# Optimization experiments

Hardware: AMD Instinct MI355X
Metric: run time of the kernel (lower is better)

The kernel has to match this reference:

```python
import jax, jax.numpy as jnp
import numpy as np

N_VEH, N_PED = 16, 16
DV, DP = 40, 24            # vehicle / pedestrian slot obs dims
N = N_VEH + N_PED          # 32 agents
E, H = 128, 4              # embed_dim, num_heads
DH = E // H                # head_dim = 32
B = 4096
OBS = N_VEH * DV + N_PED * DP + N  # 1056


def setup_inputs() -> dict:
    key = jax.random.key(0)
    ks = jax.random.split(key, 12)
    s = lambda fan_in: 1.0 / np.sqrt(fan_in)
    inp = {
        "global_obs": jax.random.uniform(ks[0], (B, OBS), dtype=jnp.float32),
        # per-type projectors (stored as (in, out) so x @ W + b)
        "Wv": jax.random.uniform(ks[1], (DV, E), jnp.float32, -s(DV), s(DV)),
        "bv": jax.random.uniform(ks[2], (E,), jnp.float32, -s(DV), s(DV)),
        "Wp": jax.random.uniform(ks[3], (DP, E), jnp.float32, -s(DP), s(DP)),
        "bp": jax.random.uniform(ks[4], (E,), jnp.float32, -s(DP), s(DP)),
        # GAT layer 0 / 1: w (E, H*DH), a_src / a_dst (H, DH)
        "w0": jax.random.normal(ks[5], (E, H * DH), jnp.float32) * s(E),
        "asrc0": jax.random.normal(ks[6], (H, DH), jnp.float32) * s(DH),
        "adst0": jax.random.normal(ks[7], (H, DH), jnp.float32) * s(DH),
        "w1": jax.random.normal(ks[8], (E, H * DH), jnp.float32) * s(E),
        "asrc1": jax.random.normal(ks[9], (H, DH), jnp.float32) * s(DH),
        "adst1": jax.random.normal(ks[10], (H, DH), jnp.float32) * s(DH),
    }
    return inp


def _gat(x, alive, w, a_src, a_dst):
    # x: (B,N,E), alive: (B,N) in {0,1}
    b, n, _ = x.shape
    h = (x @ w).reshape(b, n, H, DH)                       # (B,N,H,DH)
    alpha_src = jnp.einsum("bnhd,hd->bnh", h, a_src)       # (B,N,H)
    alpha_dst = jnp.einsum("bnhd,hd->bnh", h, a_dst)
    e = alpha_src[:, :, None, :] + alpha_dst[:, None, :, :]  # (B,Ni,Nj,H)
    e = jnp.where(e > 0, e, 0.2 * e)                       # LeakyReLU(0.2)
    key_mask = alive[:, None, :, None] >= 0.5              # mask over j
    e = jnp.where(key_mask, e, -jnp.inf)
    attn = jax.nn.softmax(e, axis=2)                       # softmax over keys j
    attn = jnp.nan_to_num(attn)
    out = jnp.einsum("bijh,bjhd->bihd", attn, h)           # weighted aggregate
    return out.reshape(b, n, H * DH)                       # concat heads


def reference(global_obs, Wv, bv, Wp, bp, w0, asrc0, adst0, w1, asrc1, adst1):
    b = global_obs.shape[0]
    veh = global_obs[:, : N_VEH * DV].reshape(b, N_VEH, DV)
    ped = global_obs[:, N_VEH * DV : N_VEH * DV + N_PED * DP].reshape(b, N_PED, DP)
    alive_raw = global_obs[:, -N:]
    tokens = jnp.concatenate([veh @ Wv + bv, ped @ Wp + bp], axis=1)  # (B,N,E)
    alive = (alive_raw >= 0.5).astype(jnp.float32)
    all_dead = jnp.sum(alive, axis=1, keepdims=True) < 0.5
    alive = jnp.where(all_dead, jnp.ones_like(alive), alive)
    x = tokens
    for (w, a_s, a_d) in ((w0, asrc0, adst0), (w1, asrc1, adst1)):
        x = jax.nn.elu(_gat(x, alive, w, a_s, a_d))
    aw = alive[:, :, None]
    pooled = jnp.sum(x * aw, axis=1) / jnp.clip(jnp.sum(aw, axis=1), 1.0)
    return pooled
```

## Files before the change

### kernel.cpp

```cpp
#include <hip/hip_runtime.h>


#define NTOK 32
#define EMB  128
#define OBSL 1056
#define XSTR 136
#define HSTR 40
#define TILE 5120

typedef __attribute__((ext_vector_type(8))) short  short8;
typedef __attribute__((ext_vector_type(4))) float  floatx4;
typedef __attribute__((ext_vector_type(2))) unsigned uint2v;

__device__ __forceinline__ short f2bf(float f) {
  union { float f; unsigned u; } v; v.f = f;
  unsigned r = (v.u + 0x7fffu + ((v.u >> 16) & 1u)) >> 16;
  return (short)(unsigned short)r;
}
__device__ __forceinline__ unsigned pk2(float a, float b) {
  unsigned r; asm("v_cvt_pk_bf16_f32 %0, %1, %2" : "=v"(r) : "v"(a), "v"(b)); return r;
}
__device__ __forceinline__ float exp2_hw(float x) {
#if __has_builtin(__builtin_amdgcn_exp2f)
  return __builtin_amdgcn_exp2f(x);
#else
  return exp2f(x);
#endif
}
__device__ __forceinline__ float rcp_hw(float x) {
#if __has_builtin(__builtin_amdgcn_rcpf)
  return __builtin_amdgcn_rcpf(x);
#else
  return 1.0f / x;
#endif
}
__device__ __forceinline__ float elu1(float v) { return v > 0.f ? v : __expf(v) - 1.f; }
__device__ __forceinline__ floatx4 mfma16(short8 a, short8 b, floatx4 c) {
  return __builtin_amdgcn_mfma_f32_16x16x32_bf16(a, b, c, 0, 0, 0);
}

__global__ void prep_weights(const float* __restrict__ Wv, const float* __restrict__ Wp,
                             const float* __restrict__ w0, const float* __restrict__ w1,
                             short* __restrict__ ws) {
  int idx = blockIdx.x * 256 + threadIdx.x;
  if (idx < 8192) {
    int e = idx >> 6, k = idx & 63;
    float v = (k < 40) ? Wv[(size_t)k * EMB + e] : Wp[(size_t)(k - 40) * EMB + e];
    ws[idx] = f2bf(v);
  } else if (idx < 24576) {
    int t = idx - 8192; int e = t >> 7, k = t & 127;
    ws[idx] = f2bf(w0[(size_t)k * EMB + e]);
  } else {
    int t = idx - 24576; int e = t >> 7, k = t & 127;
    ws[idx] = f2bf(w1[(size_t)k * EMB + e]);
  }
}

__global__ __launch_bounds__(256, 6) void gnn_fused(
    const float* __restrict__ obs,
    const float* __restrict__ bv, const float* __restrict__ bp,
    const float* __restrict__ as0, const float* __restrict__ ad0,
    const float* __restrict__ as1, const float* __restrict__ ad1,
    const short* __restrict__ wsb,
    float* __restrict__ out)
{
  __shared__ __align__(16) short s_t[TILE];

  const int tid  = threadIdx.x;
  const int lane = tid & 63;
  const int wv   = tid >> 6;
  const int col  = lane & 15;
  const int quad = lane >> 4;
  const int b    = blockIdx.x;

  const float* orow = obs + (size_t)b * OBSL;
  short* xbase = s_t;
  short* hbase = &s_t[wv * 1280];
  const short8  z8 = {0,0,0,0,0,0,0,0};
  const floatx4 fz = {0.f,0.f,0.f,0.f};

  float flag; float invc;
  {
    float araw = (lane < NTOK) ? orow[1024 + lane] : 0.f;
    bool alv = (lane < NTOK) && (araw >= 0.5f);
    unsigned long long m = __ballot(alv);
    int cnt = __popcll(m);
    flag = alv ? 1.f : 0.f;
    if (cnt == 0) { flag = (lane < NTOK) ? 1.f : 0.f; cnt = NTOK; }
    invc = 1.f / (float)cnt;
  }
  const float alvI0 = __shfl(flag, col);
  const float alvI1 = __shfl(flag, 16 + col);

  {
    int c = wv * 64 + lane;
    *(short8*)&xbase[(c >> 3) * XSTR + (c & 7) * 8] = z8;
  }
  __syncthreads();
  {
    int i4 = wv * 64 + lane;
    float4 v = *(const float4*)&orow[i4 * 4];
    int r, k;
    if (i4 < 160) { r = (i4 * 205) >> 11;  k = (i4 - r * 10) * 4; }
    else { int t2 = i4 - 160; int q6 = (t2 * 171) >> 10; r = 16 + q6; k = 40 + (t2 - q6 * 6) * 4; }
    uint2v u; u.x = pk2(v.x, v.y); u.y = pk2(v.z, v.w);
    *(uint2v*)&xbase[r * XSTR + k] = u;
  }
  __syncthreads();

  {
    short8 Bxin[2][2];
    #pragma unroll
    for (int nt = 0; nt < 2; ++nt)
      #pragma unroll
      for (int kt = 0; kt < 2; ++kt)
        Bxin[nt][kt] = *(const short8*)&xbase[(nt * 16 + col) * XSTR + kt * 32 + quad * 8];
    __syncthreads();
    const short* embT = wsb;
    #pragma unroll
    for (int mi = 0; mi < 2; ++mi) {
      const int mtE = wv * 2 + mi;
      short8 A0 = *(const short8*)&embT[(mtE * 16 + col) * 64 + quad * 8];
      short8 A1 = *(const short8*)&embT[(mtE * 16 + col) * 64 + 32 + quad * 8];
      float4 bv4 = *(const float4*)&bv[mtE * 16 + quad * 4];
      float4 bp4 = *(const float4*)&bp[mtE * 16 + quad * 4];
      #pragma unroll
      for (int nt = 0; nt < 2; ++nt) {
        floatx4 acc = fz;
        acc = mfma16(A0, Bxin[nt][0], acc);
        acc = mfma16(A1, Bxin[nt][1], acc);
        float4 bb = nt ? bp4 : bv4;
        uint2v u; u.x = pk2(acc[0] + bb.x, acc[1] + bb.y); u.y = pk2(acc[2] + bb.z, acc[3] + bb.w);
        *(uint2v*)&xbase[(nt * 16 + col) * XSTR + mtE * 16 + quad * 4] = u;
      }
    }
  }

  for (int L = 0; L < 2; ++L) {
    const short* wT  = wsb + 8192 + L * 16384;
    const float* gas = L ? as1 : as0;
    const float* gad = L ? ad1 : ad0;

    __syncthreads();

    floatx4 acc[2][2];
    #pragma unroll
    for (int mi = 0; mi < 2; ++mi) { acc[mi][0] = fz; acc[mi][1] = fz; }
    #pragma unroll
    for (int kt = 0; kt < 4; ++kt) {
      short8 B0 = *(const short8*)&xbase[(col) * XSTR + kt * 32 + quad * 8];
      short8 B1 = *(const short8*)&xbase[(16 + col) * XSTR + kt * 32 + quad * 8];
      #pragma unroll
      for (int mi = 0; mi < 2; ++mi) {
        const int mt = wv * 2 + mi;
        short8 A = *(const short8*)&wT[(mt * 16 + col) * 128 + kt * 32 + quad * 8];
        acc[mi][0] = mfma16(A, B0, acc[mi][0]);
        acc[mi][1] = mfma16(A, B1, acc[mi][1]);
      }
    }

    float psrc[2], pdst[2];
    psrc[0] = 0.f; psrc[1] = 0.f; pdst[0] = 0.f; pdst[1] = 0.f;
    #pragma unroll
    for (int mi = 0; mi < 2; ++mi) {
      const int mt = wv * 2 + mi;
      float4 cs = *(const float4*)&gas[mt * 16 + quad * 4];
      float4 cd = *(const float4*)&gad[mt * 16 + quad * 4];
      #pragma unroll
      for (int nt = 0; nt < 2; ++nt) {
        floatx4 a = acc[mi][nt];
        psrc[nt] += a[0]*cs.x + a[1]*cs.y + a[2]*cs.z + a[3]*cs.w;
        pdst[nt] += a[0]*cd.x + a[1]*cd.y + a[2]*cd.z + a[3]*cd.w;
      }
    }
    __syncthreads();

    #pragma unroll
    for (int mi = 0; mi < 2; ++mi) {
      const int rowloc = mi * 16 + quad * 4;
      #pragma unroll
      for (int nt = 0; nt < 2; ++nt) {
        floatx4 a = acc[mi][nt];
        unsigned u01 = pk2(a[0], a[1]);
        unsigned u23 = pk2(a[2], a[3]);
        unsigned short* hrow = (unsigned short*)&hbase[rowloc * HSTR + nt * 16 + col];
        hrow[0]        = (unsigned short)u01;
        hrow[HSTR]     = (unsigned short)(u01 >> 16);
        hrow[2 * HSTR] = (unsigned short)u23;
        hrow[3 * HSTR] = (unsigned short)(u23 >> 16);
      }
    }

    #pragma unroll
    for (int nt = 0; nt < 2; ++nt) {
      float vs = psrc[nt]; vs += __shfl_xor(vs, 16); vs += __shfl_xor(vs, 32);
      psrc[nt] = vs * 1.44269504088896340736f;
      float vd = pdst[nt]; vd += __shfl_xor(vd, 16); vd += __shfl_xor(vd, 32);
      pdst[nt] = vd * 1.44269504088896340736f;
    }

    float alv8[8];
    #pragma unroll
    for (int jj = 0; jj < 8; ++jj) alv8[jj] = __shfl(flag, quad * 8 + jj);

    short8 pf[2];
    {
      float vsel = (quad >> 1) ? pdst[1] : pdst[0];
      float ad8[8];
      #pragma unroll
      for (int jj = 0; jj < 8; ++jj) {
        float v = __shfl(vsel, ((quad >> 1) << 5) + ((quad & 1) << 3) + jj);
        ad8[jj] = (alv8[jj] >= 0.5f) ? v : -1e30f;
      }
      #pragma unroll
      for (int ii = 0; ii < 2; ++ii) {
        float ai = psrc[ii];
        float ev[8]; float sum = 0.f;
        #pragma unroll
        for (int jj = 0; jj < 8; ++jj) {
          float e = ai + ad8[jj];
          e = fmaxf(e, 0.2f * e);
          float p = exp2_hw(e);
          ev[jj] = p; sum += p;
        }
        sum += __shfl_xor(sum, 16);
        sum += __shfl_xor(sum, 32);
        float inv = rcp_hw(sum);
        union { unsigned u4[4]; short8 s; } pu;
        #pragma unroll
        for (int p2 = 0; p2 < 4; ++p2) pu.u4[p2] = pk2(ev[2*p2] * inv, ev[2*p2+1] * inv);
        pf[ii] = pu.s;
      }
    }

    short8 Ah[2];
    #pragma unroll
    for (int mt2 = 0; mt2 < 2; ++mt2)
      Ah[mt2] = *(const short8*)&hbase[(mt2 * 16 + col) * HSTR + quad * 8];
    if (L == 0) __syncthreads();

    #pragma unroll
    for (int mt2 = 0; mt2 < 2; ++mt2) {
      floatx4 po[2];
      #pragma unroll
      for (int nt = 0; nt < 2; ++nt) {
        po[nt] = mfma16(Ah[mt2], pf[nt], fz);
      }
      const int ecol = wv * 32 + mt2 * 16 + quad * 4;
      if (L == 0) {
        #pragma unroll
        for (int nt = 0; nt < 2; ++nt) {
          uint2v u;
          u.x = pk2(elu1(po[nt][0]), elu1(po[nt][1]));
          u.y = pk2(elu1(po[nt][2]), elu1(po[nt][3]));
          *(uint2v*)&xbase[(nt * 16 + col) * XSTR + ecol] = u;
        }
      } else {
        #pragma unroll
        for (int r = 0; r < 4; ++r) {
          float s = elu1(po[0][r]) * alvI0 + elu1(po[1][r]) * alvI1;
          s += __shfl_xor(s, 1); s += __shfl_xor(s, 2);
          s += __shfl_xor(s, 4); s += __shfl_xor(s, 8);
          if (col == 0) out[(size_t)b * EMB + ecol + r] = s * invc;
        }
      }
    }
  }
}

extern "C" void kernel_launch(void* const* d_in, const int* in_sizes, int n_in,
                              void* d_out, int out_size, void* d_ws, size_t ws_size,
                              hipStream_t stream) {
  const float* obs = (const float*)d_in[0];
  const float* Wv  = (const float*)d_in[1];
  const float* bv  = (const float*)d_in[2];
  const float* Wp  = (const float*)d_in[3];
  const float* bp  = (const float*)d_in[4];
  const float* w0  = (const float*)d_in[5];
  const float* as0 = (const float*)d_in[6];
  const float* ad0 = (const float*)d_in[7];
  const float* w1  = (const float*)d_in[8];
  const float* as1 = (const float*)d_in[9];
  const float* ad1 = (const float*)d_in[10];
  float* out = (float*)d_out;
  short* wsb = (short*)d_ws;

  int Bn = in_sizes[0] / OBSL;
  prep_weights<<<160, 256, 0, stream>>>(Wv, Wp, w0, w1, wsb);
  gnn_fused<<<Bn, 256, 0, stream>>>(obs, bv, bp, as0, ad0, as1, ad1, wsb, out);
}
```

Measured before the change: 130.2 us.

## Process two batch samples per block to reuse weight fragments

Each block now handles two batch rows with a doubled shared tile, so the weight A-fragments loaded from global memory are reused across both samples in the embedding and GAT matmuls. Alive flags become a 32-bit mask in place of per-lane floats and shuffles, and the zero-fill only touches the padding regions. The grid is halved, which raises register and LDS pressure per block and may lower occupancy under the 6-blocks launch bound. It also assumes an even batch size.

```diff
diff --git a/kernel.cpp b/kernel.cpp
--- a/kernel.cpp
+++ b/kernel.cpp
@@ -64,57 +64,62 @@
     const short* __restrict__ wsb,
     float* __restrict__ out)
 {
-  __shared__ __align__(16) short s_t[TILE];
+  __shared__ __align__(16) short s_t[2][TILE];
 
   const int tid  = threadIdx.x;
   const int lane = tid & 63;
   const int wv   = tid >> 6;
   const int col  = lane & 15;
   const int quad = lane >> 4;
-  const int b    = blockIdx.x;
-
-  const float* orow = obs + (size_t)b * OBSL;
-  short* xbase = s_t;
-  short* hbase = &s_t[wv * 1280];
+  const size_t b0 = (size_t)blockIdx.x * 2;
+
   const short8  z8 = {0,0,0,0,0,0,0,0};
   const floatx4 fz = {0.f,0.f,0.f,0.f};
 
-  float flag; float invc;
-  {
+  unsigned m32[2]; float invc[2];
+  #pragma unroll
+  for (int j = 0; j < 2; ++j) {
+    const float* orow = obs + (b0 + j) * OBSL;
     float araw = (lane < NTOK) ? orow[1024 + lane] : 0.f;
     bool alv = (lane < NTOK) && (araw >= 0.5f);
     unsigned long long m = __ballot(alv);
     int cnt = __popcll(m);
-    flag = alv ? 1.f : 0.f;
-    if (cnt == 0) { flag = (lane < NTOK) ? 1.f : 0.f; cnt = NTOK; }
-    invc = 1.f / (float)cnt;
-  }
-  const float alvI0 = __shfl(flag, col);
-  const float alvI1 = __shfl(flag, 16 + col);
+    unsigned mm = (unsigned)m;
+    if (cnt == 0) { mm = 0xFFFFFFFFu; cnt = NTOK; }
+    m32[j] = mm; invc[j] = 1.f / (float)cnt;
+  }
 
   {
-    int c = wv * 64 + lane;
-    *(short8*)&xbase[(c >> 3) * XSTR + (c & 7) * 8] = z8;
-  }
-  __syncthreads();
-  {
+    int idx = tid; int r = -1, k = 0;
+    if (idx < 48)       { r = (idx * 171) >> 9;  k = 40 + (idx - r * 3) * 8; }
+    else if (idx < 128) { int t2 = idx - 48; int q5 = (t2 * 205) >> 10; r = 16 + q5; k = (t2 - q5 * 5) * 8; }
+    if (r >= 0) {
+      *(short8*)&s_t[0][r * XSTR + k] = z8;
+      *(short8*)&s_t[1][r * XSTR + k] = z8;
+    }
+  }
+  #pragma unroll
+  for (int j = 0; j < 2; ++j) {
+    const float* orow = obs + (b0 + j) * OBSL;
     int i4 = wv * 64 + lane;
     float4 v = *(const float4*)&orow[i4 * 4];
     int r, k;
     if (i4 < 160) { r = (i4 * 205) >> 11;  k = (i4 - r * 10) * 4; }
     else { int t2 = i4 - 160; int q6 = (t2 * 171) >> 10; r = 16 + q6; k = 40 + (t2 - q6 * 6) * 4; }
     uint2v u; u.x = pk2(v.x, v.y); u.y = pk2(v.z, v.w);
-    *(uint2v*)&xbase[r * XSTR + k] = u;
+    *(uint2v*)&s_t[j][r * XSTR + k] = u;
   }
   __syncthreads();
 
   {
-    short8 Bxin[2][2];
-    #pragma unroll
-    for (int nt = 0; nt < 2; ++nt)
-      #pragma unroll
-      for (int kt = 0; kt < 2; ++kt)
-        Bxin[nt][kt] = *(const short8*)&xbase[(nt * 16 + col) * XSTR + kt * 32 + quad * 8];
+    short8 Bxin[2][2][2];
+    #pragma unroll
+    for (int j = 0; j < 2; ++j)
+      #pragma unroll
+      for (int nt = 0; nt < 2; ++nt)
+        #pragma unroll
+        for (int kt = 0; kt < 2; ++kt)
+          Bxin[j][nt][kt] = *(const short8*)&s_t[j][(nt * 16 + col) * XSTR + kt * 32 + quad * 8];
     __syncthreads();
     const short* embT = wsb;
     #pragma unroll
@@ -125,14 +130,16 @@
       float4 bv4 = *(const float4*)&bv[mtE * 16 + quad * 4];
       float4 bp4 = *(const float4*)&bp[mtE * 16 + quad * 4];
       #pragma unroll
-      for (int nt = 0; nt < 2; ++nt) {
-        floatx4 acc = fz;
-        acc = mfma16(A0, Bxin[nt][0], acc);
-        acc = mfma16(A1, Bxin[nt][1], acc);
-        float4 bb = nt ? bp4 : bv4;
-        uint2v u; u.x = pk2(acc[0] + bb.x, acc[1] + bb.y); u.y = pk2(acc[2] + bb.z, acc[3] + bb.w);
-        *(uint2v*)&xbase[(nt * 16 + col) * XSTR + mtE * 16 + quad * 4] = u;
-      }
+      for (int j = 0; j < 2; ++j)
+        #pragma unroll
+        for (int nt = 0; nt < 2; ++nt) {
+          floatx4 acc = fz;
+          acc = mfma16(A0, Bxin[j][nt][0], acc);
+          acc = mfma16(A1, Bxin[j][nt][1], acc);
+          float4 bb = nt ? bp4 : bv4;
+          uint2v u; u.x = pk2(acc[0] + bb.x, acc[1] + bb.y); u.y = pk2(acc[2] + bb.z, acc[3] + bb.w);
+          *(uint2v*)&s_t[j][(nt * 16 + col) * XSTR + mtE * 16 + quad * 4] = u;
+        }
     }
   }
 
@@ -143,78 +150,88 @@
 
     __syncthreads();
 
-    floatx4 acc[2][2];
-    #pragma unroll
-    for (int mi = 0; mi < 2; ++mi) { acc[mi][0] = fz; acc[mi][1] = fz; }
+    floatx4 acc[2][2][2];
+    #pragma unroll
+    for (int j = 0; j < 2; ++j)
+      #pragma unroll
+      for (int mi = 0; mi < 2; ++mi) { acc[j][mi][0] = fz; acc[j][mi][1] = fz; }
     #pragma unroll
     for (int kt = 0; kt < 4; ++kt) {
-      short8 B0 = *(const short8*)&xbase[(col) * XSTR + kt * 32 + quad * 8];
-      short8 B1 = *(const short8*)&xbase[(16 + col) * XSTR + kt * 32 + quad * 8];
-      #pragma unroll
-      for (int mi = 0; mi < 2; ++mi) {
-        const int mt = wv * 2 + mi;
-        short8 A = *(const short8*)&wT[(mt * 16 + col) * 128 + kt * 32 + quad * 8];
-        acc[mi][0] = mfma16(A, B0, acc[mi][0]);
-        acc[mi][1] = mfma16(A, B1, acc[mi][1]);
-      }
-    }
-
-    float psrc[2], pdst[2];
-    psrc[0] = 0.f; psrc[1] = 0.f; pdst[0] = 0.f; pdst[1] = 0.f;
+      #pragma unroll
+      for (int j = 0; j < 2; ++j) {
+        short8 B0 = *(const short8*)&s_t[j][(col) * XSTR + kt * 32 + quad * 8];
+        short8 B1 = *(const short8*)&s_t[j][(16 + col) * XSTR + kt * 32 + quad * 8];
+        #pragma unroll
+        for (int mi = 0; mi < 2; ++mi) {
+          const int mt = wv * 2 + mi;
+          short8 A = *(const short8*)&wT[(mt * 16 + col) * 128 + kt * 32 + quad * 8];
+          acc[j][mi][0] = mfma16(A, B0, acc[j][mi][0]);
+          acc[j][mi][1] = mfma16(A, B1, acc[j][mi][1]);
+        }
+      }
+    }
+
+    float psrc[2][2], pdst[2][2];
+    #pragma unroll
+    for (int j = 0; j < 2; ++j) { psrc[j][0]=0.f; psrc[j][1]=0.f; pdst[j][0]=0.f; pdst[j][1]=0.f; }
     #pragma unroll
     for (int mi = 0; mi < 2; ++mi) {
       const int mt = wv * 2 + mi;
       float4 cs = *(const float4*)&gas[mt * 16 + quad * 4];
       float4 cd = *(const float4*)&gad[mt * 16 + quad * 4];
       #pragma unroll
+      for (int j = 0; j < 2; ++j)
+        #pragma unroll
+        for (int nt = 0; nt < 2; ++nt) {
+          floatx4 a = acc[j][mi][nt];
+          psrc[j][nt] += a[0]*cs.x + a[1]*cs.y + a[2]*cs.z + a[3]*cs.w;
+          pdst[j][nt] += a[0]*cd.x + a[1]*cd.y + a[2]*cd.z + a[3]*cd.w;
+        }
+    }
+    __syncthreads();
+
+    #pragma unroll
+    for (int j = 0; j < 2; ++j)
+      #pragma unroll
+      for (int mi = 0; mi < 2; ++mi) {
+        const int rowloc = mi * 16 + quad * 4;
+        #pragma unroll
+        for (int nt = 0; nt < 2; ++nt) {
+          floatx4 a = acc[j][mi][nt];
+          unsigned u01 = pk2(a[0], a[1]);
+          unsigned u23 = pk2(a[2], a[3]);
+          unsigned short* hrow = (unsigned short*)&s_t[j][wv * 1280 + rowloc * HSTR + nt * 16 + col];
+          hrow[0]        = (unsigned short)u01;
+          hrow[HSTR]     = (unsigned short)(u01 >> 16);
+          hrow[2 * HSTR] = (unsigned short)u23;
+          hrow[3 * HSTR] = (unsigned short)(u23 >> 16);
+        }
+      }
+
+    #pragma unroll
+    for (int j = 0; j < 2; ++j)
+      #pragma unroll
       for (int nt = 0; nt < 2; ++nt) {
-        floatx4 a = acc[mi][nt];
-        psrc[nt] += a[0]*cs.x + a[1]*cs.y + a[2]*cs.z + a[3]*cs.w;
-        pdst[nt] += a[0]*cd.x + a[1]*cd.y + a[2]*cd.z + a[3]*cd.w;
-      }
-    }
-    __syncthreads();
-
-    #pragma unroll
-    for (int mi = 0; mi < 2; ++mi) {
-      const int rowloc = mi * 16 + quad * 4;
-      #pragma unroll
-      for (int nt = 0; nt < 2; ++nt) {
-        floatx4 a = acc[mi][nt];
-        unsigned u01 = pk2(a[0], a[1]);
-        unsigned u23 = pk2(a[2], a[3]);
-        unsigned short* hrow = (unsigned short*)&hbase[rowloc * HSTR + nt * 16 + col];
-        hrow[0]        = (unsigned short)u01;
-        hrow[HSTR]     = (unsigned short)(u01 >> 16);
-        hrow[2 * HSTR] = (unsigned short)u23;
-        hrow[3 * HSTR] = (unsigned short)(u23 >> 16);
-      }
-    }
-
-    #pragma unroll
-    for (int nt = 0; nt < 2; ++nt) {
-      float vs = psrc[nt]; vs += __shfl_xor(vs, 16); vs += __shfl_xor(vs, 32);
-      psrc[nt] = vs * 1.44269504088896340736f;
-      float vd = pdst[nt]; vd += __shfl_xor(vd, 16); vd += __shfl_xor(vd, 32);
-      pdst[nt] = vd * 1.44269504088896340736f;
-    }
-
-    float alv8[8];
-    #pragma unroll
-    for (int jj = 0; jj < 8; ++jj) alv8[jj] = __shfl(flag, quad * 8 + jj);
-
-    short8 pf[2];
-    {
-      float vsel = (quad >> 1) ? pdst[1] : pdst[0];
+        float vs = psrc[j][nt]; vs += __shfl_xor(vs, 16); vs += __shfl_xor(vs, 32);
+        psrc[j][nt] = vs * 1.44269504088896340736f;
+        float vd = pdst[j][nt]; vd += __shfl_xor(vd, 16); vd += __shfl_xor(vd, 32);
+        pdst[j][nt] = vd * 1.44269504088896340736f;
+      }
+
+    short8 pf[2][2];
+    #pragma unroll
+    for (int j = 0; j < 2; ++j) {
+      float vsel = (quad >> 1) ? pdst[j][1] : pdst[j][0];
       float ad8[8];
       #pragma unroll
       for (int jj = 0; jj < 8; ++jj) {
         float v = __shfl(vsel, ((quad >> 1) << 5) + ((quad & 1) << 3) + jj);
-        ad8[jj] = (alv8[jj] >= 0.5f) ? v : -1e30f;
+        bool alive = (m32[j] >> (quad * 8 + jj)) & 1u;
+        ad8[jj] = alive ? v : -1e30f;
       }
       #pragma unroll
       for (int ii = 0; ii < 2; ++ii) {
-        float ai = psrc[ii];
+        float ai = psrc[j][ii];
         float ev[8]; float sum = 0.f;
         #pragma unroll
         for (int jj = 0; jj < 8; ++jj) {
@@ -229,39 +246,46 @@
         union { unsigned u4[4]; short8 s; } pu;
         #pragma unroll
         for (int p2 = 0; p2 < 4; ++p2) pu.u4[p2] = pk2(ev[2*p2] * inv, ev[2*p2+1] * inv);
-        pf[ii] = pu.s;
-      }
-    }
-
-    short8 Ah[2];
-    #pragma unroll
-    for (int mt2 = 0; mt2 < 2; ++mt2)
-      Ah[mt2] = *(const short8*)&hbase[(mt2 * 16 + col) * HSTR + quad * 8];
+        pf[j][ii] = pu.s;
+      }
+    }
+
+    short8 Ah[2][2];
+    #pragma unroll
+    for (int j = 0; j < 2; ++j)
+      #pragma unroll
+      for (int mt2 = 0; mt2 < 2; ++mt2)
+        Ah[j][mt2] = *(const short8*)&s_t[j][wv * 1280 + (mt2 * 16 + col) * HSTR + quad * 8];
     if (L == 0) __syncthreads();
 
     #pragma unroll
-    for (int mt2 = 0; mt2 < 2; ++mt2) {
-      floatx4 po[2];
-      #pragma unroll
-      for (int nt = 0; nt < 2; ++nt) {
-        po[nt] = mfma16(Ah[mt2], pf[nt], fz);
-      }
-      const int ecol = wv * 32 + mt2 * 16 + quad * 4;
-      if (L == 0) {
+    for (int j = 0; j < 2; ++j) {
+      #pragma unroll
+      for (int mt2 = 0; mt2 < 2; ++mt2) {
+        floatx4 po[2];
         #pragma unroll
         for (int nt = 0; nt < 2; ++nt) {
-          uint2v u;
-          u.x = pk2(elu1(po[nt][0]), elu1(po[nt][1]));
-          u.y = pk2(elu1(po[nt][2]), elu1(po[nt][3]));
-          *(uint2v*)&xbase[(nt * 16 + col) * XSTR + ecol] = u;
-        }
-      } else {
-        #pragma unroll
-        for (int r = 0; r < 4; ++r) {
-          float s = elu1(po[0][r]) * alvI0 + elu1(po[1][r]) * alvI1;
-          s += __shfl_xor(s, 1); s += __shfl_xor(s, 2);
-          s += __shfl_xor(s, 4); s += __shfl_xor(s, 8);
-          if (col == 0) out[(size_t)b * EMB + ecol + r] = s * invc;
+          po[nt] = mfma16(Ah[j][mt2], pf[j][nt], fz);
+        }
+        const int ecol = wv * 32 + mt2 * 16 + quad * 4;
+        if (L == 0) {
+          #pragma unroll
+          for (int nt = 0; nt < 2; ++nt) {
+            uint2v u;
+            u.x = pk2(elu1(po[nt][0]), elu1(po[nt][1]));
+            u.y = pk2(elu1(po[nt][2]), elu1(po[nt][3]));
+            *(uint2v*)&s_t[j][(nt * 16 + col) * XSTR + ecol] = u;
+          }
+        } else {
+          float aI0 = ((m32[j] >> col) & 1u) ? 1.f : 0.f;
+          float aI1 = ((m32[j] >> (16 + col)) & 1u) ? 1.f : 0.f;
+          #pragma unroll
+          for (int r = 0; r < 4; ++r) {
+            float s = elu1(po[0][r]) * aI0 + elu1(po[1][r]) * aI1;
+            s += __shfl_xor(s, 1); s += __shfl_xor(s, 2);
+            s += __shfl_xor(s, 4); s += __shfl_xor(s, 8);
+            if (col == 0) out[(b0 + j) * EMB + ecol + r] = s * invc[j];
+          }
         }
       }
     }
@@ -287,5 +311,5 @@
 
   int Bn = in_sizes[0] / OBSL;
   prep_weights<<<160, 256, 0, stream>>>(Wv, Wp, w0, w1, wsb);
-  gnn_fused<<<Bn, 256, 0, stream>>>(obs, bv, bp, as0, ad0, as1, ad1, wsb, out);
-}
+  gnn_fused<<<Bn / 2, 256, 0, stream>>>(obs, bv, bp, as0, ad0, as1, ad1, wsb, out);
+}
```

Result: no change. 128.8 us (-1.1%).

## Process two batch rows per block with separate x/h shared buffers

Applied to the files above, without the earlier changes.

Each block now loops over two samples, which halves the grid and amortizes block launch overhead. Shared memory is split into separate x and h buffers, so the h-tile writes no longer alias x and one barrier per layer can be dropped. Only the padding columns are zeroed, and the alive flags are kept as a 32-bit bitmask instead of shuffled floats. The two samples are handled one after the other, so per-block latency roughly doubles and fewer blocks are available to hide it; Bn/2 also assumes an even batch size.

```diff
diff --git a/kernel.cpp b/kernel.cpp
--- a/kernel.cpp
+++ b/kernel.cpp
@@ -6,7 +6,6 @@
 #define OBSL 1056
 #define XSTR 136
 #define HSTR 40
-#define TILE 5120
 
 typedef __attribute__((ext_vector_type(8))) short  short8;
 typedef __attribute__((ext_vector_type(4))) float  floatx4;
@@ -64,204 +63,206 @@
     const short* __restrict__ wsb,
     float* __restrict__ out)
 {
-  __shared__ __align__(16) short s_t[TILE];
+  __shared__ __align__(16) short s_x[32 * XSTR];
+  __shared__ __align__(16) short s_h[4 * 32 * HSTR];
 
   const int tid  = threadIdx.x;
   const int lane = tid & 63;
   const int wv   = tid >> 6;
   const int col  = lane & 15;
   const int quad = lane >> 4;
-  const int b    = blockIdx.x;
-
-  const float* orow = obs + (size_t)b * OBSL;
-  short* xbase = s_t;
-  short* hbase = &s_t[wv * 1280];
+
+  short* hbase = &s_h[wv * 1280];
   const short8  z8 = {0,0,0,0,0,0,0,0};
   const floatx4 fz = {0.f,0.f,0.f,0.f};
 
-  float flag; float invc;
-  {
-    float araw = (lane < NTOK) ? orow[1024 + lane] : 0.f;
-    bool alv = (lane < NTOK) && (araw >= 0.5f);
-    unsigned long long m = __ballot(alv);
-    int cnt = __popcll(m);
-    flag = alv ? 1.f : 0.f;
-    if (cnt == 0) { flag = (lane < NTOK) ? 1.f : 0.f; cnt = NTOK; }
-    invc = 1.f / (float)cnt;
-  }
-  const float alvI0 = __shfl(flag, col);
-  const float alvI1 = __shfl(flag, 16 + col);
-
-  {
-    int c = wv * 64 + lane;
-    *(short8*)&xbase[(c >> 3) * XSTR + (c & 7) * 8] = z8;
-  }
-  __syncthreads();
-  {
-    int i4 = wv * 64 + lane;
-    float4 v = *(const float4*)&orow[i4 * 4];
-    int r, k;
-    if (i4 < 160) { r = (i4 * 205) >> 11;  k = (i4 - r * 10) * 4; }
-    else { int t2 = i4 - 160; int q6 = (t2 * 171) >> 10; r = 16 + q6; k = 40 + (t2 - q6 * 6) * 4; }
-    uint2v u; u.x = pk2(v.x, v.y); u.y = pk2(v.z, v.w);
-    *(uint2v*)&xbase[r * XSTR + k] = u;
-  }
-  __syncthreads();
-
-  {
-    short8 Bxin[2][2];
-    #pragma unroll
-    for (int nt = 0; nt < 2; ++nt)
-      #pragma unroll
-      for (int kt = 0; kt < 2; ++kt)
-        Bxin[nt][kt] = *(const short8*)&xbase[(nt * 16 + col) * XSTR + kt * 32 + quad * 8];
+  for (int j = 0; j < 2; ++j) {
+    const size_t b = (size_t)blockIdx.x * 2 + j;
+    const float* orow = obs + b * OBSL;
+
     __syncthreads();
-    const short* embT = wsb;
-    #pragma unroll
-    for (int mi = 0; mi < 2; ++mi) {
-      const int mtE = wv * 2 + mi;
-      short8 A0 = *(const short8*)&embT[(mtE * 16 + col) * 64 + quad * 8];
-      short8 A1 = *(const short8*)&embT[(mtE * 16 + col) * 64 + 32 + quad * 8];
-      float4 bv4 = *(const float4*)&bv[mtE * 16 + quad * 4];
-      float4 bp4 = *(const float4*)&bp[mtE * 16 + quad * 4];
-      #pragma unroll
-      for (int nt = 0; nt < 2; ++nt) {
-        floatx4 acc = fz;
-        acc = mfma16(A0, Bxin[nt][0], acc);
-        acc = mfma16(A1, Bxin[nt][1], acc);
-        float4 bb = nt ? bp4 : bv4;
-        uint2v u; u.x = pk2(acc[0] + bb.x, acc[1] + bb.y); u.y = pk2(acc[2] + bb.z, acc[3] + bb.w);
-        *(uint2v*)&xbase[(nt * 16 + col) * XSTR + mtE * 16 + quad * 4] = u;
-      }
-    }
-  }
-
-  for (int L = 0; L < 2; ++L) {
-    const short* wT  = wsb + 8192 + L * 16384;
-    const float* gas = L ? as1 : as0;
-    const float* gad = L ? ad1 : ad0;
-
+
+    unsigned m32; float invc;
+    {
+      float araw = (lane < NTOK) ? orow[1024 + lane] : 0.f;
+      bool alv = (lane < NTOK) && (araw >= 0.5f);
+      unsigned long long m = __ballot(alv);
+      int cnt = __popcll(m);
+      unsigned mm = (unsigned)m;
+      if (cnt == 0) { mm = 0xFFFFFFFFu; cnt = NTOK; }
+      m32 = mm; invc = 1.f / (float)cnt;
+    }
+
+    {
+      int idx = tid; int r = -1, k = 0;
+      if (idx < 48)       { r = (idx * 171) >> 9;  k = 40 + (idx - r * 3) * 8; }
+      else if (idx < 128) { int t2 = idx - 48; int q5 = (t2 * 205) >> 10; r = 16 + q5; k = (t2 - q5 * 5) * 8; }
+      if (r >= 0) *(short8*)&s_x[r * XSTR + k] = z8;
+    }
+    {
+      int i4 = wv * 64 + lane;
+      float4 v = *(const float4*)&orow[i4 * 4];
+      int r, k;
+      if (i4 < 160) { r = (i4 * 205) >> 11;  k = (i4 - r * 10) * 4; }
+      else { int t2 = i4 - 160; int q6 = (t2 * 171) >> 10; r = 16 + q6; k = 40 + (t2 - q6 * 6) * 4; }
+      uint2v u; u.x = pk2(v.x, v.y); u.y = pk2(v.z, v.w);
+      *(uint2v*)&s_x[r * XSTR + k] = u;
+    }
     __syncthreads();
 
-    floatx4 acc[2][2];
-    #pragma unroll
-    for (int mi = 0; mi < 2; ++mi) { acc[mi][0] = fz; acc[mi][1] = fz; }
-    #pragma unroll
-    for (int kt = 0; kt < 4; ++kt) {
-      short8 B0 = *(const short8*)&xbase[(col) * XSTR + kt * 32 + quad * 8];
-      short8 B1 = *(const short8*)&xbase[(16 + col) * XSTR + kt * 32 + quad * 8];
+    {
+      short8 Bxin[2][2];
+      #pragma unroll
+      for (int nt = 0; nt < 2; ++nt)
+        #pragma unroll
+        for (int kt = 0; kt < 2; ++kt)
+          Bxin[nt][kt] = *(const short8*)&s_x[(nt * 16 + col) * XSTR + kt * 32 + quad * 8];
+      __syncthreads();
+      const short* embT = wsb;
+      #pragma unroll
+      for (int mi = 0; mi < 2; ++mi) {
+        const int mtE = wv * 2 + mi;
+        short8 A0 = *(const short8*)&embT[(mtE * 16 + col) * 64 + quad * 8];
+        short8 A1 = *(const short8*)&embT[(mtE * 16 + col) * 64 + 32 + quad * 8];
+        float4 bv4 = *(const float4*)&bv[mtE * 16 + quad * 4];
+        float4 bp4 = *(const float4*)&bp[mtE * 16 + quad * 4];
+        #pragma unroll
+        for (int nt = 0; nt < 2; ++nt) {
+          floatx4 acc = fz;
+          acc = mfma16(A0, Bxin[nt][0], acc);
+          acc = mfma16(A1, Bxin[nt][1], acc);
+          float4 bb = nt ? bp4 : bv4;
+          uint2v u; u.x = pk2(acc[0] + bb.x, acc[1] + bb.y); u.y = pk2(acc[2] + bb.z, acc[3] + bb.w);
+          *(uint2v*)&s_x[(nt * 16 + col) * XSTR + mtE * 16 + quad * 4] = u;
+        }
+      }
+    }
+
+    for (int L = 0; L < 2; ++L) {
+      const short* wT  = wsb + 8192 + L * 16384;
+      const float* gas = L ? as1 : as0;
+      const float* gad = L ? ad1 : ad0;
+
+      __syncthreads();
+
+      floatx4 acc[2][2];
+      #pragma unroll
+      for (int mi = 0; mi < 2; ++mi) { acc[mi][0] = fz; acc[mi][1] = fz; }
+      #pragma unroll
+      for (int kt = 0; kt < 4; ++kt) {
+        short8 B0 = *(const short8*)&s_x[(col) * XSTR + kt * 32 + quad * 8];
+        short8 B1 = *(const short8*)&s_x[(16 + col) * XSTR + kt * 32 + quad * 8];
+        #pragma unroll
+        for (int mi = 0; mi < 2; ++mi) {
+          const int mt = wv * 2 + mi;
+          short8 A = *(const short8*)&wT[(mt * 16 + col) * 128 + kt * 32 + quad * 8];
+          acc[mi][0] = mfma16(A, B0, acc[mi][0]);
+          acc[mi][1] = mfma16(A, B1, acc[mi][1]);
+        }
+      }
+
+      float psrc[2], pdst[2];
+      psrc[0] = 0.f; psrc[1] = 0.f; pdst[0] = 0.f; pdst[1] = 0.f;
       #pragma unroll
       for (int mi = 0; mi < 2; ++mi) {
         const int mt = wv * 2 + mi;
-        short8 A = *(const short8*)&wT[(mt * 16 + col) * 128 + kt * 32 + quad * 8];
-        acc[mi][0] = mfma16(A, B0, acc[mi][0]);
-        acc[mi][1] = mfma16(A, B1, acc[mi][1]);
-      }
-    }
-
-    float psrc[2], pdst[2];
-    psrc[0] = 0.f; psrc[1] = 0.f; pdst[0] = 0.f; pdst[1] = 0.f;
-    #pragma unroll
-    for (int mi = 0; mi < 2; ++mi) {
-      const int mt = wv * 2 + mi;
-      float4 cs = *(const float4*)&gas[mt * 16 + quad * 4];
-      float4 cd = *(const float4*)&gad[mt * 16 + quad * 4];
+        float4 cs = *(const float4*)&gas[mt * 16 + quad * 4];
+        float4 cd = *(const float4*)&gad[mt * 16 + quad * 4];
+        #pragma unroll
+        for (int nt = 0; nt < 2; ++nt) {
+          floatx4 a = acc[mi][nt];
+          psrc[nt] += a[0]*cs.x + a[1]*cs.y + a[2]*cs.z + a[3]*cs.w;
+          pdst[nt] += a[0]*cd.x + a[1]*cd.y + a[2]*cd.z + a[3]*cd.w;
+        }
+      }
+
+      #pragma unroll
+      for (int mi = 0; mi < 2; ++mi) {
+        const int rowloc = mi * 16 + quad * 4;
+        #pragma unroll
+        for (int nt = 0; nt < 2; ++nt) {
+          floatx4 a = acc[mi][nt];
+          unsigned u01 = pk2(a[0], a[1]);
+          unsigned u23 = pk2(a[2], a[3]);
+          unsigned short* hrow = (unsigned short*)&hbase[rowloc * HSTR + nt * 16 + col];
+          hrow[0]        = (unsigned short)u01;
+          hrow[HSTR]     = (unsigned short)(u01 >> 16);
+          hrow[2 * HSTR] = (unsigned short)u23;
+          hrow[3 * HSTR] = (unsigned short)(u23 >> 16);
+        }
+      }
+
       #pragma unroll
       for (int nt = 0; nt < 2; ++nt) {
-        floatx4 a = acc[mi][nt];
-        psrc[nt] += a[0]*cs.x + a[1]*cs.y + a[2]*cs.z + a[3]*cs.w;
-        pdst[nt] += a[0]*cd.x + a[1]*cd.y + a[2]*cd.z + a[3]*cd.w;
-      }
-    }
-    __syncthreads();
-
-    #pragma unroll
-    for (int mi = 0; mi < 2; ++mi) {
-      const int rowloc = mi * 16 + quad * 4;
-      #pragma unroll
-      for (int nt = 0; nt < 2; ++nt) {
-        floatx4 a = acc[mi][nt];
-        unsigned u01 = pk2(a[0], a[1]);
-        unsigned u23 = pk2(a[2], a[3]);
-        unsigned short* hrow = (unsigned short*)&hbase[rowloc * HSTR + nt * 16 + col];
-        hrow[0]        = (unsigned short)u01;
-        hrow[HSTR]     = (unsigned short)(u01 >> 16);
-        hrow[2 * HSTR] = (unsigned short)u23;
-        hrow[3 * HSTR] = (unsigned short)(u23 >> 16);
-      }
-    }
-
-    #pragma unroll
-    for (int nt = 0; nt < 2; ++nt) {
-      float vs = psrc[nt]; vs += __shfl_xor(vs, 16); vs += __shfl_xor(vs, 32);
-      psrc[nt] = vs * 1.44269504088896340736f;
-      float vd = pdst[nt]; vd += __shfl_xor(vd, 16); vd += __shfl_xor(vd, 32);
-      pdst[nt] = vd * 1.44269504088896340736f;
-    }
-
-    float alv8[8];
-    #pragma unroll
-    for (int jj = 0; jj < 8; ++jj) alv8[jj] = __shfl(flag, quad * 8 + jj);
-
-    short8 pf[2];
-    {
-      float vsel = (quad >> 1) ? pdst[1] : pdst[0];
-      float ad8[8];
-      #pragma unroll
-      for (int jj = 0; jj < 8; ++jj) {
-        float v = __shfl(vsel, ((quad >> 1) << 5) + ((quad & 1) << 3) + jj);
-        ad8[jj] = (alv8[jj] >= 0.5f) ? v : -1e30f;
-      }
-      #pragma unroll
-      for (int ii = 0; ii < 2; ++ii) {
-        float ai = psrc[ii];
-        float ev[8]; float sum = 0.f;
+        float vs = psrc[nt]; vs += __shfl_xor(vs, 16); vs += __shfl_xor(vs, 32);
+        psrc[nt] = vs * 1.44269504088896340736f;
+        float vd = pdst[nt]; vd += __shfl_xor(vd, 16); vd += __shfl_xor(vd, 32);
+        pdst[nt] = vd * 1.44269504088896340736f;
+      }
+
+      short8 pf[2];
+      {
+        float vsel = (quad >> 1) ? pdst[1] : pdst[0];
+        float ad8[8];
         #pragma unroll
         for (int jj = 0; jj < 8; ++jj) {
-          float e = ai + ad8[jj];
-          e = fmaxf(e, 0.2f * e);
-          float p = exp2_hw(e);
-          ev[jj] = p; sum += p;
-        }
-        sum += __shfl_xor(sum, 16);
-        sum += __shfl_xor(sum, 32);
-        float inv = rcp_hw(sum);
-        union { unsigned u4[4]; short8 s; } pu;
-        #pragma unroll
-        for (int p2 = 0; p2 < 4; ++p2) pu.u4[p2] = pk2(ev[2*p2] * inv, ev[2*p2+1] * inv);
-        pf[ii] = pu.s;
-      }
-    }
-
-    short8 Ah[2];
-    #pragma unroll
-    for (int mt2 = 0; mt2 < 2; ++mt2)
-      Ah[mt2] = *(const short8*)&hbase[(mt2 * 16 + col) * HSTR + quad * 8];
-    if (L == 0) __syncthreads();
-
-    #pragma unroll
-    for (int mt2 = 0; mt2 < 2; ++mt2) {
-      floatx4 po[2];
-      #pragma unroll
-      for (int nt = 0; nt < 2; ++nt) {
-        po[nt] = mfma16(Ah[mt2], pf[nt], fz);
-      }
-      const int ecol = wv * 32 + mt2 * 16 + quad * 4;
-      if (L == 0) {
-        #pragma unroll
-        for (int nt = 0; nt < 2; ++nt) {
-          uint2v u;
-          u.x = pk2(elu1(po[nt][0]), elu1(po[nt][1]));
-          u.y = pk2(elu1(po[nt][2]), elu1(po[nt][3]));
-          *(uint2v*)&xbase[(nt * 16 + col) * XSTR + ecol] = u;
-        }
-      } else {
-        #pragma unroll
-        for (int r = 0; r < 4; ++r) {
-          float s = elu1(po[0][r]) * alvI0 + elu1(po[1][r]) * alvI1;
-          s += __shfl_xor(s, 1); s += __shfl_xor(s, 2);
-          s += __shfl_xor(s, 4); s += __shfl_xor(s, 8);
-          if (col == 0) out[(size_t)b * EMB + ecol + r] = s * invc;
+          float v = __shfl(vsel, ((quad >> 1) << 5) + ((quad & 1) << 3) + jj);
+          bool alive = (m32 >> (quad * 8 + jj)) & 1u;
+          ad8[jj] = alive ? v : -1e30f;
+        }
+        #pragma unroll
+        for (int ii = 0; ii < 2; ++ii) {
+          float ai = psrc[ii];
+          float ev[8]; float sum = 0.f;
+          #pragma unroll
+          for (int jj = 0; jj < 8; ++jj) {
+            float e = ai + ad8[jj];
+            e = fmaxf(e, 0.2f * e);
+            float p = exp2_hw(e);
+            ev[jj] = p; sum += p;
+          }
+          sum += __shfl_xor(sum, 16);
+          sum += __shfl_xor(sum, 32);
+          float inv = rcp_hw(sum);
+          union { unsigned u4[4]; short8 s; } pu;
+          #pragma unroll
+          for (int p2 = 0; p2 < 4; ++p2) pu.u4[p2] = pk2(ev[2*p2] * inv, ev[2*p2+1] * inv);
+          pf[ii] = pu.s;
+        }
+      }
+
+      short8 Ah[2];
+      #pragma unroll
+      for (int mt2 = 0; mt2 < 2; ++mt2)
+        Ah[mt2] = *(const short8*)&hbase[(mt2 * 16 + col) * HSTR + quad * 8];
+      if (L == 0) __syncthreads();
+
+      #pragma unroll
+      for (int mt2 = 0; mt2 < 2; ++mt2) {
+        floatx4 po[2];
+        #pragma unroll
+        for (int nt = 0; nt < 2; ++nt) {
+          po[nt] = mfma16(Ah[mt2], pf[nt], fz);
+        }
+        const int ecol = wv * 32 + mt2 * 16 + quad * 4;
+        if (L == 0) {
+          #pragma unroll
+          for (int nt = 0; nt < 2; ++nt) {
+            uint2v u;
+            u.x = pk2(elu1(po[nt][0]), elu1(po[nt][1]));
+            u.y = pk2(elu1(po[nt][2]), elu1(po[nt][3]));
+            *(uint2v*)&s_x[(nt * 16 + col) * XSTR + ecol] = u;
+          }
+        } else {
+          float aI0 = ((m32 >> col) & 1u) ? 1.f : 0.f;
+          float aI1 = ((m32 >> (16 + col)) & 1u) ? 1.f : 0.f;
+          #pragma unroll
+          for (int r = 0; r < 4; ++r) {
+            float s = elu1(po[0][r]) * aI0 + elu1(po[1][r]) * aI1;
+            s += __shfl_xor(s, 1); s += __shfl_xor(s, 2);
+            s += __shfl_xor(s, 4); s += __shfl_xor(s, 8);
+            if (col == 0) out[b * EMB + ecol + r] = s * invc;
+          }
         }
       }
     }
@@ -287,5 +288,5 @@
 
   int Bn = in_sizes[0] / OBSL;
   prep_weights<<<160, 256, 0, stream>>>(Wv, Wp, w0, w1, wsb);
-  gnn_fused<<<Bn, 256, 0, stream>>>(obs, bv, bp, as0, ad0, as1, ad1, wsb, out);
-}
+  gnn_fused<<<Bn / 2, 256, 0, stream>>>(obs, bv, bp, as0, ad0, as1, ad1, wsb, out);
+}
```

Result: slower. 188.9 us (+45.0%).
